# Kernel tuning notes

Hardware: AMD Instinct MI355X
Metric: run time of the kernel (lower is better)

## Reference

```python
import jax, jax.numpy as jnp
import numpy as np

TEMPERATURE = 0.5  # init kwarg; forward's temperature arg is unused in the original

def _l2norm(x, eps=1e-12):
    # matches F.normalize(dim=-1)
    n = jnp.sqrt(jnp.sum(x * x, axis=-1, keepdims=True))
    return x / jnp.maximum(n, eps)

def setup_inputs() -> dict:
    key = jax.random.key(0)
    k1, k2 = jax.random.split(key)
    h1 = jax.random.normal(k1, (8192, 128), dtype=jnp.float32)
    h2 = jax.random.normal(k2, (8192, 128), dtype=jnp.float32)
    return {"h1": h1, "h2": h2}

def reference(h1, h2):
    t = TEMPERATURE
    h1n = _l2norm(h1)
    h2n = _l2norm(h2)
    h = jnp.concatenate([h1n, h2n], axis=0)              # [2N, d]
    sim = jnp.exp(jnp.matmul(h, h.T) / t)                # [2N, 2N]
    # masked_select of off-diagonal then row-sum == full row-sum minus diagonal
    denom = jnp.sum(sim, axis=-1) - jnp.diagonal(sim)    # [2N]
    pos = jnp.exp(jnp.sum(h1n * h2n, axis=-1) / t)       # [N]
    pos = jnp.concatenate([pos, pos], axis=0)            # [2N]
    loss = -jnp.log(pos / denom)
    return jnp.mean(loss)
```

## Files before the change

kernel.cpp:

```cpp
#include <hip/hip_runtime.h>
#include <hip/hip_bf16.h>

#define N_ROWS 8192
#define DIM    128
#define TWO_N  16384
#define CSPLIT 32
#define COLS_PER_BLOCK (TWO_N / CSPLIT)
#define CT 32
#define NT (COLS_PER_BLOCK / CT)
#define EXP_TWO 7.38905609893065f
#define H_SCALE 1.6986436f

typedef __attribute__((ext_vector_type(8))) short short8;
typedef __attribute__((ext_vector_type(4))) float float4v;

__device__ inline void async_copy16(const void* g, void* l) {
  __builtin_amdgcn_global_load_lds(
      (const __attribute__((address_space(1))) void*)g,
      (__attribute__((address_space(3))) void*)l, 16, 0, 0);
}

__device__ inline float fast_exp2(float x) {
#if __has_builtin(__builtin_amdgcn_exp2f)
  return __builtin_amdgcn_exp2f(x);
#else
  return exp2f(x);
#endif
}

__global__ __launch_bounds__(256) void norm_kernel(
    const float* __restrict__ h1, const float* __restrict__ h2,
    __hip_bfloat16* __restrict__ Hb, float* __restrict__ posdot,
    float* __restrict__ rowsum) {
  if (threadIdx.x < 8) rowsum[blockIdx.x * 8 + threadIdx.x] = 0.0f;

  int lane = threadIdx.x & 63;
  int w    = threadIdx.x >> 6;
  int row  = blockIdx.x * 4 + w;

  const float2* p1 = (const float2*)(h1 + (size_t)row * DIM);
  const float2* p2 = (const float2*)(h2 + (size_t)row * DIM);
  float2 v1 = p1[lane];
  float2 v2 = p2[lane];

  float ss1 = v1.x * v1.x + v1.y * v1.y;
  float ss2 = v2.x * v2.x + v2.y * v2.y;
  #pragma unroll
  for (int m = 32; m; m >>= 1) {
    ss1 += __shfl_xor(ss1, m);
    ss2 += __shfl_xor(ss2, m);
  }
  float inv1 = 1.0f / fmaxf(sqrtf(ss1), 1e-12f);
  float inv2 = 1.0f / fmaxf(sqrtf(ss2), 1e-12f);

  float ax = v1.x * inv1, ay = v1.y * inv1;
  float bx = v2.x * inv2, by = v2.y * inv2;

  float pd = ax * bx + ay * by;
  #pragma unroll
  for (int m = 32; m; m >>= 1) pd += __shfl_xor(pd, m);

  __hip_bfloat162* o1 = (__hip_bfloat162*)(Hb + (size_t)row * DIM);
  __hip_bfloat162* o2 = (__hip_bfloat162*)(Hb + (size_t)(row + N_ROWS) * DIM);
  __hip_bfloat162 t1, t2;
  t1.x = __float2bfloat16(ax * H_SCALE); t1.y = __float2bfloat16(ay * H_SCALE);
  t2.x = __float2bfloat16(bx * H_SCALE); t2.y = __float2bfloat16(by * H_SCALE);
  o1[lane] = t1;
  o2[lane] = t2;

  if (lane == 0) posdot[row] = pd;
}

__global__ __launch_bounds__(256, 2) void ntx_main(
    const __hip_bfloat16* __restrict__ Hb, float* __restrict__ rowsum) {
  __shared__ short smem[512 * 8];
  const short* H = (const short*)Hb;

  int tid  = threadIdx.x;
  int lane = tid & 63;
  int w    = tid >> 6;
  int q    = lane >> 4;
  int m    = lane & 15;

  int rowbase = blockIdx.x * 256 + w * 64;
  int colbase = blockIdx.y * COLS_PER_BLOCK;

  short8 a[4][4];
  #pragma unroll
  for (int r = 0; r < 4; ++r)
    #pragma unroll
    for (int s = 0; s < 4; ++s)
      a[r][s] = *(const short8*)(H + (size_t)(rowbase + r * 16 + m) * DIM + s * 32 + q * 8);

  float rowacc[4][4];
  #pragma unroll
  for (int r = 0; r < 4; ++r)
    #pragma unroll
    for (int i = 0; i < 4; ++i) rowacc[r][i] = 0.0f;

  for (int ct = 0; ct < NT; ++ct) {
    int j0 = colbase + ct * CT;
    #pragma unroll
    for (int rr = 0; rr < 2; ++rr) {
      int i   = rr * 256 + tid;
      int c   = i >> 8;
      int s   = (i >> 6) & 3;
      int l15 = i & 15;
      int lq  = (i >> 4) & 3;
      const short* g = H + (size_t)(j0 + c * 16 + l15) * DIM + s * 32 + lq * 8;
      async_copy16(g, (void*)&smem[i * 8]);
    }
    __syncthreads();

    #pragma unroll
    for (int c = 0; c < 2; ++c) {
      short8 b[4];
      #pragma unroll
      for (int s = 0; s < 4; ++s)
        b[s] = *(const short8*)&smem[(c * 256 + s * 64 + lane) * 8];
      #pragma unroll
      for (int r = 0; r < 4; ++r) {
        float4v acc = {0.f, 0.f, 0.f, 0.f};
        #pragma unroll
        for (int s = 0; s < 4; ++s)
          acc = __builtin_amdgcn_mfma_f32_16x16x32_bf16(a[r][s], b[s], acc, 0, 0, 0);
        #pragma unroll
        for (int i = 0; i < 4; ++i)
          rowacc[r][i] += fast_exp2(acc[i]);
      }
    }
    __syncthreads();
  }

  #pragma unroll
  for (int r = 0; r < 4; ++r)
    #pragma unroll
    for (int i = 0; i < 4; ++i) {
      float v = rowacc[r][i];
      v += __shfl_xor(v, 1);
      v += __shfl_xor(v, 2);
      v += __shfl_xor(v, 4);
      v += __shfl_xor(v, 8);
      rowacc[r][i] = v;
    }
  if (m == 0) {
    #pragma unroll
    for (int r = 0; r < 4; ++r)
      #pragma unroll
      for (int i = 0; i < 4; ++i)
        atomicAdd(&rowsum[rowbase + r * 16 + q * 4 + i], rowacc[r][i]);
  }
}

__global__ __launch_bounds__(1024) void finalize(
    const float* __restrict__ rowsum, const float* __restrict__ posdot,
    float* __restrict__ out) {
  __shared__ float red[32];
  int tid = threadIdx.x;
  float ld = 0.0f, pp = 0.0f;
  for (int i = tid; i < TWO_N; i += 1024) ld += logf(rowsum[i] - EXP_TWO);
  for (int i = tid; i < N_ROWS; i += 1024) pp += posdot[i];
  #pragma unroll
  for (int m = 32; m; m >>= 1) {
    ld += __shfl_xor(ld, m);
    pp += __shfl_xor(pp, m);
  }
  if ((tid & 63) == 0) {
    red[tid >> 6] = ld;
    red[16 + (tid >> 6)] = pp;
  }
  __syncthreads();
  if (tid == 0) {
    float tl = 0.0f, tp = 0.0f;
    #pragma unroll
    for (int i = 0; i < 16; ++i) { tl += red[i]; tp += red[16 + i]; }
    *out = (tl - 4.0f * tp) / (float)TWO_N;
  }
}

extern "C" void kernel_launch(void* const* d_in, const int* in_sizes, int n_in,
                              void* d_out, int out_size, void* d_ws, size_t ws_size,
                              hipStream_t stream) {
  const float* h1 = (const float*)d_in[0];
  const float* h2 = (const float*)d_in[1];
  char* ws = (char*)d_ws;

  __hip_bfloat16* Hb = (__hip_bfloat16*)ws;
  float* rowsum      = (float*)(ws + 4194304);
  float* posdot      = (float*)(ws + 4194304 + 65536);
  float* out         = (float*)d_out;

  norm_kernel<<<N_ROWS / 4, 256, 0, stream>>>(h1, h2, Hb, posdot, rowsum);
  ntx_main<<<dim3(TWO_N / 256, CSPLIT), 256, 0, stream>>>(Hb, rowsum);
  finalize<<<1, 1024, 0, stream>>>(rowsum, posdot, out);
}
```

Before: 139.3 us.

## Double-buffer LDS column tiles to overlap async loads with MFMA compute

```diff
diff --git a/kernel.cpp b/kernel.cpp
--- a/kernel.cpp
+++ b/kernel.cpp
@@ -73,7 +73,7 @@
 
 __global__ __launch_bounds__(256, 2) void ntx_main(
     const __hip_bfloat16* __restrict__ Hb, float* __restrict__ rowsum) {
-  __shared__ short smem[512 * 8];
+  __shared__ short smem[2 * 4096];
   const short* H = (const short*)Hb;
 
   int tid  = threadIdx.x;
@@ -91,6 +91,11 @@
     #pragma unroll
     for (int s = 0; s < 4; ++s)
       a[r][s] = *(const short8*)(H + (size_t)(rowbase + r * 16 + m) * DIM + s * 32 + q * 8);
+  #pragma unroll
+  for (int r = 0; r < 4; ++r)
+    #pragma unroll
+    for (int s = 0; s < 4; ++s)
+      asm volatile("" : "+v"(a[r][s]));
 
   float rowacc[4][4];
   #pragma unroll
@@ -98,26 +103,33 @@
     #pragma unroll
     for (int i = 0; i < 4; ++i) rowacc[r][i] = 0.0f;
 
+  int i0 = tid, i1 = tid + 256;
+  int c0 = i0 >> 8, s0 = (i0 >> 6) & 3, f0 = i0 & 15, q0 = (i0 >> 4) & 3;
+  int c1 = i1 >> 8, s1 = (i1 >> 6) & 3, f1 = i1 & 15, q1 = (i1 >> 4) & 3;
+  const short* ga = H + (size_t)(colbase + c0 * 16 + f0) * DIM + s0 * 32 + q0 * 8;
+  const short* gb = H + (size_t)(colbase + c1 * 16 + f1) * DIM + s1 * 32 + q1 * 8;
+
+  async_copy16(ga, (void*)&smem[i0 * 8]);
+  async_copy16(gb, (void*)&smem[i1 * 8]);
+  __syncthreads();
+
+  int buf = 0;
   for (int ct = 0; ct < NT; ++ct) {
-    int j0 = colbase + ct * CT;
-    #pragma unroll
-    for (int rr = 0; rr < 2; ++rr) {
-      int i   = rr * 256 + tid;
-      int c   = i >> 8;
-      int s   = (i >> 6) & 3;
-      int l15 = i & 15;
-      int lq  = (i >> 4) & 3;
-      const short* g = H + (size_t)(j0 + c * 16 + l15) * DIM + s * 32 + lq * 8;
-      async_copy16(g, (void*)&smem[i * 8]);
+    if (ct + 1 < NT) {
+      ga += CT * DIM;
+      gb += CT * DIM;
+      int d = (buf ^ 1) * 4096;
+      async_copy16(ga, (void*)&smem[d + i0 * 8]);
+      async_copy16(gb, (void*)&smem[d + i1 * 8]);
     }
-    __syncthreads();
-
+
+    const short* bsrc = &smem[buf * 4096];
     #pragma unroll
     for (int c = 0; c < 2; ++c) {
       short8 b[4];
       #pragma unroll
       for (int s = 0; s < 4; ++s)
-        b[s] = *(const short8*)&smem[(c * 256 + s * 64 + lane) * 8];
+        b[s] = *(const short8*)&bsrc[(c * 256 + s * 64 + lane) * 8];
       #pragma unroll
       for (int r = 0; r < 4; ++r) {
         float4v acc = {0.f, 0.f, 0.f, 0.f};
@@ -130,6 +142,7 @@
       }
     }
     __syncthreads();
+    buf ^= 1;
   }
 
   #pragma unroll
```

Result: faster. 135.8 us (-2.5%).
